# Performance work log

Hardware: AMD Instinct MI355X
Metric: run time of the kernel (lower is better)

## Reference

```python
import jax, jax.numpy as jnp
from jax import lax
import numpy as np

D_MODEL = 1024; N_HEADS = 16; D_K = 64; D_FF = 4096
D_STATE = 16; D_CONV = 4; D_INNER = 2048; EPS = 1e-5
BATCH = 2; SEQ = 2048


def _ln(x, g, b):
    m = x.mean(-1, keepdims=True)
    v = ((x - m) ** 2).mean(-1, keepdims=True)
    return (x - m) * lax.rsqrt(v + EPS) * g + b


def setup_inputs() -> dict:
    key = jax.random.key(0)
    ks = jax.random.split(key, 12)
    rn = lambda k, sh, s=0.02: jax.random.normal(k, sh, jnp.float32) * s
    return {
        'x': jax.random.normal(ks[0], (BATCH, SEQ, D_MODEL), jnp.float32),
        'ln1_g': jnp.ones(D_MODEL), 'ln1_b': jnp.zeros(D_MODEL),
        'Wq': rn(ks[1], (D_MODEL, D_MODEL)), 'bq': jnp.zeros(D_MODEL),
        'Wk': rn(ks[2], (D_MODEL, D_MODEL)), 'bk': jnp.zeros(D_MODEL),
        'Wv': rn(ks[3], (D_MODEL, D_MODEL)), 'bv': jnp.zeros(D_MODEL),
        'Wo': rn(ks[4], (D_MODEL, D_MODEL)), 'bo': jnp.zeros(D_MODEL),
        'ln2_g': jnp.ones(D_MODEL), 'ln2_b': jnp.zeros(D_MODEL),
        'in_w': rn(ks[5], (D_MODEL, 2 * D_INNER)), 'in_b': jnp.zeros(2 * D_INNER),
        'conv_w': rn(ks[6], (D_INNER, 1, D_CONV), 0.2), 'conv_b': jnp.zeros(D_INNER),
        'xp_w': rn(ks[7], (D_INNER, 2 * D_STATE)), 'xp_b': jnp.zeros(2 * D_STATE),
        'dt': rn(ks[8], (D_INNER,), 0.1), 'A': rn(ks[9], (D_STATE, D_STATE), 0.1),
        'Dp': jnp.ones(D_INNER),
        'out_w': rn(ks[10], (D_INNER, D_MODEL)), 'out_b': jnp.zeros(D_MODEL),
        'ln3_g': jnp.ones(D_MODEL), 'ln3_b': jnp.zeros(D_MODEL),
        'fc1_w': rn(ks[11], (D_MODEL, D_FF)), 'fc1_b': jnp.zeros(D_FF),
        'fc2_w': rn(jax.random.fold_in(key, 99), (D_FF, D_MODEL)), 'fc2_b': jnp.zeros(D_MODEL),
    }


def reference(x, ln1_g, ln1_b, Wq, bq, Wk, bk, Wv, bv, Wo, bo, ln2_g, ln2_b,
              in_w, in_b, conv_w, conv_b, xp_w, xp_b, dt, A, Dp, out_w, out_b,
              ln3_g, ln3_b, fc1_w, fc1_b, fc2_w, fc2_b):
    Bsz, S, _ = x.shape
    # --- attention (block sliding-window mask == full causal mask) ---
    h = _ln(x, ln1_g, ln1_b)
    q = (h @ Wq + bq).reshape(Bsz, S, N_HEADS, D_K).transpose(0, 2, 1, 3)
    k = (h @ Wk + bk).reshape(Bsz, S, N_HEADS, D_K).transpose(0, 2, 1, 3)
    v = (h @ Wv + bv).reshape(Bsz, S, N_HEADS, D_K).transpose(0, 2, 1, 3)
    scores = jnp.einsum('bhqd,bhkd->bhqk', q, k) / float(D_K ** 0.5)
    causal = jnp.tril(jnp.ones((S, S), bool))
    scores = jnp.where(causal, scores, -jnp.inf)
    probs = jax.nn.softmax(scores, axis=-1)
    attn = jnp.einsum('bhqk,bhkd->bhqd', probs, v).transpose(0, 2, 1, 3).reshape(Bsz, S, D_MODEL)
    x = x + attn @ Wo + bo
    # --- Mamba-style layer ---
    h = _ln(x, ln2_g, ln2_b)
    xr = h @ in_w + in_b                      # (B,S,2*Di)
    xm, res = xr[..., :D_INNER], xr[..., D_INNER:]
    # causal depthwise conv: torch Conv1d(pad=d_conv-1)[..., :S] == left-pad conv
    xc = lax.conv_general_dilated(xm.transpose(0, 2, 1), conv_w, (1,), [(D_CONV - 1, 0)],
                                  dimension_numbers=('NCH', 'OIH', 'NCH'),
                                  feature_group_count=D_INNER)
    xm = jax.nn.silu((xc + conv_b[None, :, None]).transpose(0, 2, 1))
    xdbl = xm @ xp_w + xp_b                   # (B,S,2*d_state)
    Bm, Cm = xdbl[..., :D_STATE], xdbl[..., D_STATE:]
    # dt = exp(param)[:d_state], indexed by i % d_state per step (as in source)
    dts = jnp.exp(dt)[:D_STATE][jnp.arange(S) % D_STATE]  # (S,)
    # NOTE: the source scan never uses u = x[:,i,:] (and hence D); hs depends
    # only on dt, A, B, C — replicated faithfully here.

    def step(hst, inp):
        d_t, b_t, c_t = inp
        A_t = jnp.exp(d_t * A)                # (d_state,d_state)
        hst = jnp.tanh(hst @ A_t.T) + b_t * hst + c_t
        return hst, hst

    h0 = jnp.zeros((Bsz, D_STATE), x.dtype)
    _, hs = lax.scan(step, h0, (dts, Bm.transpose(1, 0, 2), Cm.transpose(1, 0, 2)))
    hs = hs.transpose(1, 0, 2)                # (B,S,d_state)
    y = jnp.repeat(hs, D_INNER // D_STATE, axis=-1) + res
    x = x + y @ out_w + out_b
    # --- FFN (tanh-approx GELU) ---
    h = _ln(x, ln3_g, ln3_b)
    x = x + jax.nn.gelu(h @ fc1_w + fc1_b, approximate=True) @ fc2_w + fc2_b
    return x
```

## Files before the change

kernel.cpp:

```cpp
#include <hip/hip_runtime.h>
#include <hip/hip_bf16.h>


#define SEQ     2048
#define BATCH   2
#define MROWS   4096
#define DMODEL  1024
#define DINNER  2048
#define DFF     4096
#define QKVLD   3072

typedef __attribute__((ext_vector_type(8))) short bf16x8;
typedef __attribute__((ext_vector_type(4))) float f32x4;
typedef __attribute__((ext_vector_type(2))) __fp16 f16x2;

__device__ __forceinline__ unsigned short f2b(float x){
    __hip_bfloat16 h = __float2bfloat16(x);
    return *reinterpret_cast<unsigned short*>(&h);
}
__device__ __forceinline__ float b2f(unsigned short u){
    __hip_bfloat16 h;
    *reinterpret_cast<unsigned short*>(&h) = u;
    return __bfloat162float(h);
}
__device__ __forceinline__ float gelu_f(float v){
    float u = 0.7978845608f*(v + 0.044715f*v*v*v);
    float e = __expf(2.f*u);
    float th = 1.f - 2.f*__builtin_amdgcn_rcpf(e + 1.f);
    return 0.5f*v*(1.f + th);
}
__device__ __forceinline__ void gload16(const unsigned short* g, unsigned short* l){
    __builtin_amdgcn_global_load_lds(
        (const __attribute__((address_space(1))) void*)g,
        (__attribute__((address_space(3))) void*)l, 16, 0, 0);
}
__device__ __forceinline__ void gload16f(const float* g, float* l){
    __builtin_amdgcn_global_load_lds(
        (const __attribute__((address_space(1))) void*)g,
        (__attribute__((address_space(3))) void*)l, 16, 0, 0);
}
template<int CTRL>
__device__ __forceinline__ float dppf(float x){
    int r = __builtin_amdgcn_mov_dpp(__builtin_bit_cast(int, x), CTRL, 0xf, 0xf, false);
    return __builtin_bit_cast(float, r);
}
template<int CTRL>
__device__ __forceinline__ int dppi(int x){
    return __builtin_amdgcn_mov_dpp(x, CTRL, 0xf, 0xf, false);
}
template<int CTRL>
__device__ __forceinline__ f16x2 dpp_h2(f16x2 x){
    int r = __builtin_amdgcn_mov_dpp(__builtin_bit_cast(int, x), CTRL, 0xf, 0xf, false);
    return __builtin_bit_cast(f16x2, r);
}

#if __has_builtin(__builtin_amdgcn_exp2f)
#define W_SCALE 2.8853900817779268f
__device__ __forceinline__ float exp_2s(float x){ return __builtin_amdgcn_exp2f(x); }
#else
#define W_SCALE 2.0f
__device__ __forceinline__ float exp_2s(float x){ return __expf(x); }
#endif

__device__ __forceinline__ float hdot2(f16x2 a, f16x2 b, float c){
#if __has_builtin(__builtin_amdgcn_fdot2)
    return __builtin_amdgcn_fdot2(a, b, c, false);
#else
    return c + (float)a[0]*(float)b[0] + (float)a[1]*(float)b[1];
#endif
}

__global__ __launch_bounds__(256) void transpose_cast(
    const float* __restrict__ W, unsigned short* __restrict__ Wt, int K, int N)
{
    __shared__ float t[64*65];
    int n0 = blockIdx.x*64, k0 = blockIdx.y*64;
    int c = threadIdx.x & 63, r0 = threadIdx.x >> 6;
    #pragma unroll
    for (int rr = 0; rr < 64; rr += 4)
        t[(rr+r0)*65 + c] = W[(size_t)(k0+rr+r0)*N + n0 + c];
    __syncthreads();
    #pragma unroll
    for (int rr = 0; rr < 64; rr += 4)
        Wt[(size_t)(n0+rr+r0)*K + k0 + c] = f2b(t[c*65 + rr + r0]);
}

__global__ __launch_bounds__(256) void concat_bias(
    const float* __restrict__ b0, const float* __restrict__ b1,
    const float* __restrict__ b2, float* __restrict__ o)
{
    int t = blockIdx.x*256 + threadIdx.x;
    float v = (t < 1024) ? b0[t] : (t < 2048 ? b1[t-1024] : b2[t-2048]);
    o[t] = v;
}

__global__ __launch_bounds__(256) void layernorm_bf16(
    const float* __restrict__ x, const float* __restrict__ g,
    const float* __restrict__ b, unsigned short* __restrict__ out)
{
    int row = blockIdx.x;
    const float4* xr = (const float4*)(x + (size_t)row*DMODEL);
    int tid = threadIdx.x;
    float4 xv = xr[tid];
    float s  = xv.x + xv.y + xv.z + xv.w;
    float ss = xv.x*xv.x + xv.y*xv.y + xv.z*xv.z + xv.w*xv.w;
    #pragma unroll
    for (int d = 32; d > 0; d >>= 1){ s += __shfl_xor(s,d); ss += __shfl_xor(ss,d); }
    __shared__ float sm[8];
    int wv = tid>>6, ln = tid&63;
    if (ln == 0){ sm[wv] = s; sm[4+wv] = ss; }
    __syncthreads();
    s  = sm[0]+sm[1]+sm[2]+sm[3];
    ss = sm[4]+sm[5]+sm[6]+sm[7];
    float mean = s*(1.f/DMODEL);
    float var  = ss*(1.f/DMODEL) - mean*mean;
    float rstd = rsqrtf(var + 1e-5f);
    float4 gv = ((const float4*)g)[tid];
    float4 bv = ((const float4*)b)[tid];
    ushort4 o;
    o.x = f2b((xv.x-mean)*rstd*gv.x + bv.x);
    o.y = f2b((xv.y-mean)*rstd*gv.y + bv.y);
    o.z = f2b((xv.z-mean)*rstd*gv.z + bv.z);
    o.w = f2b((xv.w-mean)*rstd*gv.w + bv.w);
    ((ushort4*)(out + (size_t)row*DMODEL))[tid] = o;
}

template<int BN, int OUT_BF16, int HAS_RES, int ACT>
__global__ __launch_bounds__(256,2) void gemm_bt(
    const unsigned short* __restrict__ A, const unsigned short* __restrict__ Bt,
    const float* __restrict__ bias, const float* __restrict__ res,
    void* __restrict__ outp, int Ndim, int Kdim)
{
    constexpr int NT = BN/32;
    constexpr int BROWS = BN/32;
    __shared__ unsigned short As[128*64];
    __shared__ unsigned short Bs[BN*64];
    int tid = threadIdx.x;
    int lane = tid & 63, wv = tid >> 6;
    int l15 = lane & 15, quad = lane >> 4;
    int m0 = blockIdx.y*128, n0 = blockIdx.x*BN;
    int mo = (wv>>1)*64, no = (wv&1)*(BN/2);
    int rsub = (lane >> 3);
    int cc8  = (lane & 7)*8;
    f32x4 zz = {0.f,0.f,0.f,0.f};
    f32x4 acc[4][NT];
    #pragma unroll
    for (int i=0;i<4;++i)
      #pragma unroll
      for (int j=0;j<NT;++j) acc[i][j] = zz;

    for (int k0 = 0; k0 < Kdim; k0 += 64){
        const unsigned short* Ab = A  + (size_t)(m0 + wv*32 + rsub)*Kdim + k0 + cc8;
        const unsigned short* Bb = Bt + (size_t)(n0 + wv*(BN/4) + rsub)*Kdim + k0 + cc8;
        #pragma unroll
        for (int i=0;i<4;++i)
            gload16(Ab + (size_t)(i*8)*Kdim, &As[(wv*32 + i*8)*64]);
        #pragma unroll
        for (int i=0;i<BROWS;++i)
            gload16(Bb + (size_t)(i*8)*Kdim, &Bs[(wv*(BN/4) + i*8)*64]);
        __syncthreads();
        #pragma unroll
        for (int kc=0;kc<2;++kc){
            bf16x8 af[4], bfr[NT];
            #pragma unroll
            for (int t=0;t<4;++t)
                af[t]  = *(const bf16x8*)(&As[(mo + t*16 + l15)*64 + kc*32 + quad*8]);
            #pragma unroll
            for (int t=0;t<NT;++t)
                bfr[t] = *(const bf16x8*)(&Bs[(no + t*16 + l15)*64 + kc*32 + quad*8]);
            #pragma unroll
            for (int mt=0;mt<4;++mt)
              #pragma unroll
              for (int nt=0;nt<NT;++nt)
                acc[mt][nt] = __builtin_amdgcn_mfma_f32_16x16x32_bf16(af[mt], bfr[nt], acc[mt][nt], 0,0,0);
        }
        __syncthreads();
    }
    #pragma unroll
    for (int mt=0;mt<4;++mt){
      #pragma unroll
      for (int nt=0;nt<NT;++nt){
        int gn = n0 + no + nt*16 + l15;
        float bval = bias[gn];
        #pragma unroll
        for (int r=0;r<4;++r){
            int gm = m0 + mo + mt*16 + quad*4 + r;
            size_t off = (size_t)gm*Ndim + gn;
            float v = acc[mt][nt][r] + bval;
            if constexpr (HAS_RES) v += res[off];
            if constexpr (ACT == 1) v = gelu_f(v);
            if constexpr (OUT_BF16) ((unsigned short*)outp)[off] = f2b(v);
            else                    ((float*)outp)[off] = v;
        }
      }
    }
}

__global__ __launch_bounds__(256) void transpose_v(
    const unsigned short* __restrict__ qkv, unsigned short* __restrict__ vT)
{
    __shared__ unsigned int t[64*33];
    int bh = blockIdx.y;
    int t0 = blockIdx.x*64;
    int tid = threadIdx.x;
    const size_t base = (size_t)(bh>>4)*SEQ*QKVLD + (size_t)(bh&15)*64 + 2*DMODEL;
    #pragma unroll
    for (int i=0;i<2;++i){
        int idx = tid + i*256;
        int r = idx>>3, cc = idx&7;
        uint4 vv = *(const uint4*)(qkv + base + (size_t)(t0+r)*QKVLD + cc*8);
        t[r*33 + cc*4 + 0] = vv.x;
        t[r*33 + cc*4 + 1] = vv.y;
        t[r*33 + cc*4 + 2] = vv.z;
        t[r*33 + cc*4 + 3] = vv.w;
    }
    __syncthreads();
    unsigned short* outb = vT + (size_t)bh*64*SEQ + t0;
    #pragma unroll
    for (int i=0;i<2;++i){
        int idx = tid + i*256;
        int d = idx>>3, cc = idx&7;
        int sh = (d&1)*16, dp = d>>1;
        unsigned int o4[4];
        #pragma unroll
        for (int j2=0;j2<4;++j2){
            unsigned int ua = t[(cc*8 + 2*j2    )*33 + dp];
            unsigned int ub = t[(cc*8 + 2*j2 + 1)*33 + dp];
            unsigned int ha = (ua >> sh) & 0xffff;
            unsigned int hb = (ub >> sh) & 0xffff;
            o4[j2] = ha | (hb << 16);
        }
        *(uint4*)(outb + (size_t)d*SEQ + cc*8) = *(uint4*)o4;
    }
}

__global__ __launch_bounds__(256,2) void attn_flash(
    const unsigned short* __restrict__ qkv, const unsigned short* __restrict__ vT,
    unsigned short* __restrict__ attn)
{
    __shared__ unsigned short Ks[128*72];
    __shared__ unsigned short Vt[64*136];
    __shared__ unsigned short Ps[64*136];
    int bh = blockIdx.y;
    int qt = (int)gridDim.x - 1 - (int)blockIdx.x;
    int q0 = qt*64;
    int tid = threadIdx.x, wv = tid>>6, lane = tid&63;
    int l15 = lane&15, quad = lane>>4;
    const size_t basei = (size_t)(bh>>4)*SEQ*QKVLD + (size_t)(bh&15)*64;
    const unsigned short* q = qkv + basei;
    const unsigned short* k = qkv + basei + DMODEL;
    const unsigned short* vTb = vT + (size_t)bh*64*SEQ;
    const size_t baseo = (size_t)(bh>>4)*SEQ*DMODEL + (size_t)(bh&15)*64;

    bf16x8 aq0 = *(const bf16x8*)(q + (size_t)(q0 + wv*16 + l15)*QKVLD + quad*8);
    bf16x8 aq1 = *(const bf16x8*)(q + (size_t)(q0 + wv*16 + l15)*QKVLD + 32 + quad*8);

    int nkt = (q0 + 191) >> 7;

    uint4 rK[4], rV[4];
    #pragma unroll
    for (int p=0;p<4;++p){
        int c = tid + p*256;
        rK[p] = *(const uint4*)(k   + (size_t)(c>>3)*QKVLD + (c&7)*8);
        rV[p] = *(const uint4*)(vTb + (size_t)(c>>4)*SEQ   + (c&15)*8);
    }

    float m_i[4], l_i[4];
    f32x4 zz = {0.f,0.f,0.f,0.f};
    f32x4 o[4];
    #pragma unroll
    for (int r=0;r<4;++r){ m_i[r] = -__builtin_inff(); l_i[r] = 0.f; }
    #pragma unroll
    for (int d=0;d<4;++d) o[d] = zz;

    for (int kt = 0; kt < nkt; ++kt){
        int t0 = kt*128;
        __syncthreads();
        #pragma unroll
        for (int p=0;p<4;++p){
            int c = tid + p*256;
            *(uint4*)(&Ks[(c>>3)*72  + (c&7)*8])  = rK[p];
            *(uint4*)(&Vt[(c>>4)*136 + (c&15)*8]) = rV[p];
        }
        __syncthreads();
        if (kt + 1 < nkt){
            int t1 = t0 + 128;
            #pragma unroll
            for (int p=0;p<4;++p){
                int c = tid + p*256;
                rK[p] = *(const uint4*)(k   + (size_t)(t1 + (c>>3))*QKVLD + (c&7)*8);
                rV[p] = *(const uint4*)(vTb + (size_t)(c>>4)*SEQ + t1 + (c&15)*8);
            }
        }

        f32x4 sc[8];
        #pragma unroll
        for (int st=0;st<8;++st){
            bf16x8 b0 = *(const bf16x8*)(&Ks[(st*16+l15)*72 + quad*8]);
            bf16x8 b1 = *(const bf16x8*)(&Ks[(st*16+l15)*72 + 32 + quad*8]);
            sc[st] = __builtin_amdgcn_mfma_f32_16x16x32_bf16(aq0, b0, zz, 0,0,0);
            sc[st] = __builtin_amdgcn_mfma_f32_16x16x32_bf16(aq1, b1, sc[st], 0,0,0);
        }
        bool diagt = (kt == nkt-1);
        float mrow[4];
        #pragma unroll
        for (int r=0;r<4;++r) mrow[r] = -__builtin_inff();
        #pragma unroll
        for (int st=0;st<8;++st)
          #pragma unroll
          for (int r=0;r<4;++r){
            float svv = sc[st][r]*0.125f;
            if (diagt && (t0 + st*16 + l15 > q0 + wv*16 + quad*4 + r))
                svv = -__builtin_inff();
            sc[st][r] = svv;
            mrow[r] = fmaxf(mrow[r], svv);
          }
        #pragma unroll
        for (int d=1; d<16; d<<=1)
          #pragma unroll
          for (int r=0;r<4;++r) mrow[r] = fmaxf(mrow[r], __shfl_xor(mrow[r], d));
        float alpha[4], rsum[4];
        #pragma unroll
        for (int r=0;r<4;++r){
            float mn = fmaxf(m_i[r], mrow[r]);
            alpha[r] = __expf(m_i[r] - mn);
            m_i[r] = mn;
        }
        #pragma unroll
        for (int st=0;st<8;++st)
          #pragma unroll
          for (int r=0;r<4;++r) sc[st][r] = __expf(sc[st][r] - m_i[r]);
        #pragma unroll
        for (int r=0;r<4;++r){
            rsum[r] = ((sc[0][r]+sc[1][r])+(sc[2][r]+sc[3][r]))
                    + ((sc[4][r]+sc[5][r])+(sc[6][r]+sc[7][r]));
        }
        #pragma unroll
        for (int d=1; d<16; d<<=1)
          #pragma unroll
          for (int r=0;r<4;++r) rsum[r] += __shfl_xor(rsum[r], d);
        #pragma unroll
        for (int r=0;r<4;++r) l_i[r] = l_i[r]*alpha[r] + rsum[r];
        #pragma unroll
        for (int st=0;st<8;++st)
          #pragma unroll
          for (int r=0;r<4;++r)
            Ps[(wv*16 + quad*4 + r)*136 + st*16 + l15] = f2b(sc[st][r]);
        #pragma unroll
        for (int d=0;d<4;++d)
          #pragma unroll
          for (int r=0;r<4;++r) o[d][r] = o[d][r]*alpha[r];

        bf16x8 ap[4];
        #pragma unroll
        for (int kch=0;kch<4;++kch)
            ap[kch] = *(const bf16x8*)(&Ps[(wv*16 + l15)*136 + kch*32 + quad*8]);
        #pragma unroll
        for (int dtile=0;dtile<4;++dtile){
            #pragma unroll
            for (int kch=0;kch<4;++kch){
                bf16x8 bv_ = *(const bf16x8*)(&Vt[(dtile*16+l15)*136 + kch*32 + quad*8]);
                o[dtile] = __builtin_amdgcn_mfma_f32_16x16x32_bf16(ap[kch], bv_, o[dtile], 0,0,0);
            }
        }
    }
    #pragma unroll
    for (int r=0;r<4;++r){
        float inv = 1.f/l_i[r];
        int gm = q0 + wv*16 + quad*4 + r;
        #pragma unroll
        for (int dtile=0;dtile<4;++dtile)
            attn[baseo + (size_t)gm*DMODEL + dtile*16 + l15] = f2b(o[dtile][r]*inv);
    }
}

__global__ __launch_bounds__(256) void conv_silu(
    const unsigned short* __restrict__ xr, const float* __restrict__ cw,
    const float* __restrict__ cb, unsigned short* __restrict__ xm2)
{
    int idx = blockIdx.x*256 + threadIdx.x;
    int r  = idx >> 10;
    int c2 = (idx & 1023)*2;
    int s  = r & (SEQ-1);
    float4 w0 = *(const float4*)(cw + c2*4);
    float4 w1 = *(const float4*)(cw + (c2+1)*4);
    float w0a[4] = {w0.x,w0.y,w0.z,w0.w};
    float w1a[4] = {w1.x,w1.y,w1.z,w1.w};
    float a0 = cb[c2], a1 = cb[c2+1];
    const unsigned short* xrow = xr + (size_t)r*DFF + c2;
    #pragma unroll
    for (int j=0;j<4;++j){
        int sp = s - 3 + j;
        if (sp >= 0){
            int off = (j-3)*DFF;
            unsigned int u = *(const unsigned int*)(xrow + off);
            a0 += w0a[j]*b2f(u & 0xffff);
            a1 += w1a[j]*b2f(u >> 16);
        }
    }
    float s0 = a0 * __builtin_amdgcn_rcpf(1.f + __expf(-a0));
    float s1 = a1 * __builtin_amdgcn_rcpf(1.f + __expf(-a1));
    unsigned int op = (unsigned int)f2b(s0) | ((unsigned int)f2b(s1) << 16);
    *(unsigned int*)(xm2 + (size_t)r*DINNER + c2) = op;
}

__global__ __launch_bounds__(256) void xp_gemm(
    const unsigned short* __restrict__ xm2, const float* __restrict__ w,
    const float* __restrict__ bias, float* __restrict__ xdbl)
{
    int tid = threadIdx.x;
    int lr = tid >> 5, n = tid & 31;
    int row = blockIdx.x*8 + lr;
    const unsigned short* ar = xm2 + (size_t)row*DINNER;
    float acc = bias[n];
    #pragma unroll 4
    for (int k2 = 0; k2 < DINNER; k2 += 2){
        unsigned int u = *(const unsigned int*)(ar + k2);
        acc += b2f(u & 0xffff)*w[k2*32 + n] + b2f(u >> 16)*w[(k2+1)*32 + n];
    }
    int nc = (n < 16) ? 2*n : 2*(n-16)+1;
    xdbl[(size_t)row*32 + nc] = acc;
}

__device__ __forceinline__ float scan_step_dot(float h, const f16x2 (&Wp)[8],
                                               float bv, float cv)
{
    float rr = dppf<0x121>(h);
    f16x2 p0 = __builtin_amdgcn_cvt_pkrtz(h, rr);
    f16x2 p1 = dpp_h2<0x122>(p0);
    f16x2 p2 = dpp_h2<0x124>(p0);
    f16x2 p3 = dpp_h2<0x126>(p0);
    f16x2 p4 = dpp_h2<0x128>(p0);
    f16x2 p5 = dpp_h2<0x12a>(p0);
    f16x2 p6 = dpp_h2<0x12c>(p0);
    f16x2 p7 = dpp_h2<0x12e>(p0);
    float a0 = hdot2(Wp[0], p0, 0.f);
    a0 = hdot2(Wp[1], p1, a0);
    a0 = hdot2(Wp[2], p2, a0);
    a0 = hdot2(Wp[3], p3, a0);
    float a1 = hdot2(Wp[4], p4, 0.f);
    a1 = hdot2(Wp[5], p5, a1);
    a1 = hdot2(Wp[6], p6, a1);
    a1 = hdot2(Wp[7], p7, a1);
    float u  = fmaf(bv, h, cv + 1.f);
    float e2 = exp_2s(a0 + a1);
    float r  = __builtin_amdgcn_rcpf(e2 + 1.f);
    return fmaf(-2.f, r, u);
}

__device__ __forceinline__ void load_bank(float2 (&bk)[16], const float* src){
    #pragma unroll
    for (int j=0;j<16;++j) bk[j] = *(const float2*)(src + (size_t)j*32);
}

__device__ __forceinline__ void compute16(const float2 (&bk)[16],
                                          const f16x2 (&Wf)[16][8],
                                          float& hn, float* hp, int lane)
{
    float h0s=0.f, h1s=0.f, h2s=0.f;
    #pragma unroll
    for (int j=0;j<16;++j){
        hn = scan_step_dot(hn, Wf[j], bk[j].x, bk[j].y);
        if ((j&3)==0)      h0s = hn;
        else if ((j&3)==1) h1s = hn;
        else if ((j&3)==2) h2s = hn;
        else if (lane < 16){
            float4 o4 = {h0s, h1s, h2s, hn};
            *(float4*)(hp + j - 3) = o4;
        }
    }
}

__global__ __launch_bounds__(128,1) void scan_k(
    const float* __restrict__ xdbl, const float* __restrict__ dt,
    const float* __restrict__ A, float* __restrict__ hsT)
{
    int tid = threadIdx.x;
    int lane = tid & 63;
    int b = tid >> 6;
    int i = lane & 15;

    int c1 = dppi<0x121>(i);
    int sj[8], tj[8];
    sj[0] = i;               tj[0] = c1;
    sj[1] = dppi<0x122>(i);  tj[1] = dppi<0x122>(c1);
    sj[2] = dppi<0x124>(i);  tj[2] = dppi<0x124>(c1);
    sj[3] = dppi<0x126>(i);  tj[3] = dppi<0x126>(c1);
    sj[4] = dppi<0x128>(i);  tj[4] = dppi<0x128>(c1);
    sj[5] = dppi<0x12a>(i);  tj[5] = dppi<0x12a>(c1);
    sj[6] = dppi<0x12c>(i);  tj[6] = dppi<0x12c>(c1);
    sj[7] = dppi<0x12e>(i);  tj[7] = dppi<0x12e>(c1);

    f16x2 Wf[16][8];
    #pragma unroll
    for (int p=0;p<16;++p){
        float dtp = __expf(dt[p]);
        #pragma unroll
        for (int jj=0;jj<8;++jj){
            float w0 = W_SCALE*__expf(dtp * A[i*16 + sj[jj]]);
            float w1 = W_SCALE*__expf(dtp * A[i*16 + tj[jj]]);
            Wf[p][jj] = __builtin_amdgcn_cvt_pkrtz(w0, w1);
        }
    }

    const float* src = xdbl + (size_t)(b*SEQ)*32 + 2*i;
    float* hp = hsT + (size_t)(b*16 + i)*SEQ;
    float2 bA[16], bB[16];
    load_bank(bA, src);
    float hn = 0.f;
    for (int bp = 0; bp < 64; ++bp){
        int t0 = bp*32;
        load_bank(bB, src + (size_t)(t0+16)*32);
        compute16(bA, Wf, hn, hp + t0, lane);
        int t2 = (bp < 63) ? (t0 + 32) : 0;
        load_bank(bA, src + (size_t)t2*32);
        compute16(bB, Wf, hn, hp + t0 + 16, lane);
    }
}

__global__ __launch_bounds__(256) void y_assemble(
    const float* __restrict__ hsT, const unsigned short* __restrict__ xr,
    unsigned short* __restrict__ y)
{
    int idx = blockIdx.x*256 + threadIdx.x;
    int r = idx >> 10;
    int c2 = (idx & 1023)*2;
    int bb = r >> 11, s = r & (SEQ-1);
    unsigned int u = *(const unsigned int*)(xr + (size_t)r*DFF + DINNER + c2);
    float h0 = hsT[(size_t)(bb*16 + (c2 >> 7))*SEQ + s];
    float y0 = h0 + b2f(u & 0xffff);
    float y1 = h0 + b2f(u >> 16);
    *(unsigned int*)(y + (size_t)r*DINNER + c2) =
        (unsigned int)f2b(y0) | ((unsigned int)f2b(y1) << 16);
}

extern "C" void kernel_launch(void* const* d_in, const int* in_sizes, int n_in,
                              void* d_out, int out_size, void* d_ws, size_t ws_size,
                              hipStream_t stream)
{
    (void)in_sizes; (void)n_in; (void)out_size; (void)ws_size;
    const float* x     = (const float*)d_in[0];
    const float* ln1_g = (const float*)d_in[1];
    const float* ln1_b = (const float*)d_in[2];
    const float* Wq    = (const float*)d_in[3];
    const float* bq    = (const float*)d_in[4];
    const float* Wk    = (const float*)d_in[5];
    const float* bk    = (const float*)d_in[6];
    const float* Wv    = (const float*)d_in[7];
    const float* bv    = (const float*)d_in[8];
    const float* Wo    = (const float*)d_in[9];
    const float* bo    = (const float*)d_in[10];
    const float* ln2_g = (const float*)d_in[11];
    const float* ln2_b = (const float*)d_in[12];
    const float* in_w  = (const float*)d_in[13];
    const float* in_b  = (const float*)d_in[14];
    const float* conv_w= (const float*)d_in[15];
    const float* conv_b= (const float*)d_in[16];
    const float* xp_w  = (const float*)d_in[17];
    const float* xp_b  = (const float*)d_in[18];
    const float* dt    = (const float*)d_in[19];
    const float* A     = (const float*)d_in[20];
    const float* out_w = (const float*)d_in[22];
    const float* out_b = (const float*)d_in[23];
    const float* ln3_g = (const float*)d_in[24];
    const float* ln3_b = (const float*)d_in[25];
    const float* fc1_w = (const float*)d_in[26];
    const float* fc1_b = (const float*)d_in[27];
    const float* fc2_w = (const float*)d_in[28];
    const float* fc2_b = (const float*)d_in[29];

    char* ws = (char*)d_ws;
    const size_t MB = 1ull << 20;
    unsigned short* qkvT = (unsigned short*)(ws + 0*MB);
    unsigned short* WoT  = (unsigned short*)(ws + 6*MB);
    unsigned short* inT  = (unsigned short*)(ws + 8*MB);
    unsigned short* outT = (unsigned short*)(ws + 16*MB);
    unsigned short* f1T  = (unsigned short*)(ws + 20*MB);
    unsigned short* f2T  = (unsigned short*)(ws + 28*MB);
    unsigned short* hbf  = (unsigned short*)(ws + 36*MB);
    float*          x2   = (float*)(ws + 44*MB);
    float*          x3   = (float*)(ws + 60*MB);
    unsigned short* qkv  = (unsigned short*)(ws + 76*MB);
    unsigned short* attnb= (unsigned short*)(ws + 100*MB);
    unsigned short* xr   = (unsigned short*)(ws + 76*MB);
    unsigned short* ffn  = (unsigned short*)(ws + 76*MB);
    unsigned short* xm2  = (unsigned short*)(ws + 108*MB);
    unsigned short* yb   = (unsigned short*)(ws + 108*MB);
    float*          xdbl = (float*)(ws + 124*MB);
    float*          hsb  = (float*)(ws + 124*MB + 512*1024);
    float*          bqkv = (float*)(ws + 125*MB);

    dim3 blk(256);
    transpose_cast<<<dim3(16,16), blk, 0, stream>>>(Wq, qkvT,              1024, 1024);
    transpose_cast<<<dim3(16,16), blk, 0, stream>>>(Wk, qkvT + 1024*1024,  1024, 1024);
    transpose_cast<<<dim3(16,16), blk, 0, stream>>>(Wv, qkvT + 2*1024*1024,1024, 1024);
    transpose_cast<<<dim3(16,16), blk, 0, stream>>>(Wo, WoT, 1024, 1024);
    transpose_cast<<<dim3(64,16), blk, 0, stream>>>(in_w, inT, 1024, 4096);
    transpose_cast<<<dim3(16,32), blk, 0, stream>>>(out_w, outT, 2048, 1024);
    transpose_cast<<<dim3(64,16), blk, 0, stream>>>(fc1_w, f1T, 1024, 4096);
    transpose_cast<<<dim3(16,64), blk, 0, stream>>>(fc2_w, f2T, 4096, 1024);
    concat_bias<<<12, blk, 0, stream>>>(bq, bk, bv, bqkv);

    layernorm_bf16<<<MROWS, blk, 0, stream>>>(x, ln1_g, ln1_b, hbf);
    gemm_bt<128,1,0,0><<<dim3(24,32), blk, 0, stream>>>(hbf, qkvT, bqkv, nullptr, qkv, QKVLD, 1024);
    transpose_v<<<dim3(32,32), blk, 0, stream>>>(qkv, hbf);
    attn_flash<<<dim3(32,32), blk, 0, stream>>>(qkv, hbf, attnb);
    gemm_bt<64,0,1,0><<<dim3(16,32), blk, 0, stream>>>(attnb, WoT, bo, x, x2, 1024, 1024);
    layernorm_bf16<<<MROWS, blk, 0, stream>>>(x2, ln2_g, ln2_b, hbf);
    gemm_bt<128,1,0,0><<<dim3(32,32), blk, 0, stream>>>(hbf, inT, in_b, nullptr, xr, 4096, 1024);
    conv_silu<<<16384, blk, 0, stream>>>(xr, conv_w, conv_b, xm2);
    xp_gemm<<<512, blk, 0, stream>>>(xm2, xp_w, xp_b, xdbl);
    scan_k<<<1, dim3(128), 0, stream>>>(xdbl, dt, A, hsb);
    y_assemble<<<16384, blk, 0, stream>>>(hsb, xr, yb);
    gemm_bt<64,0,1,0><<<dim3(16,32), blk, 0, stream>>>(yb, outT, out_b, x2, x3, 1024, 2048);
    layernorm_bf16<<<MROWS, blk, 0, stream>>>(x3, ln3_g, ln3_b, hbf);
    gemm_bt<128,1,0,1><<<dim3(32,32), blk, 0, stream>>>(hbf, f1T, fc1_b, nullptr, ffn, 4096, 1024);
    gemm_bt<64,0,1,0><<<dim3(16,32), blk, 0, stream>>>(ffn, f2T, fc2_b, x3, (float*)d_out, 1024, 4096);
}
```

Before: 938.7 us.

## Stage attention K/V with direct global-to-LDS loads into XOR-swizzled tiles

The flash-attention kernel now loads K and V^T tiles straight into LDS with global_load_lds, using an XOR swizzle instead of padded rows. This replaces the old register prefetch-then-store path and frees registers, so launch bounds rise to three blocks per CU. Scores are prescaled by log2(e) so a base-2 exponential can be used. The next tile is now loaded only after the current tile's compute, between two barriers, so overlap within a block is lost; hiding that load latency now depends on the extra occupancy.

```diff
diff --git a/kernel.cpp b/kernel.cpp
--- a/kernel.cpp
+++ b/kernel.cpp
@@ -30,11 +30,6 @@
     return 0.5f*v*(1.f + th);
 }
 __device__ __forceinline__ void gload16(const unsigned short* g, unsigned short* l){
-    __builtin_amdgcn_global_load_lds(
-        (const __attribute__((address_space(1))) void*)g,
-        (__attribute__((address_space(3))) void*)l, 16, 0, 0);
-}
-__device__ __forceinline__ void gload16f(const float* g, float* l){
     __builtin_amdgcn_global_load_lds(
         (const __attribute__((address_space(1))) void*)g,
         (__attribute__((address_space(3))) void*)l, 16, 0, 0);
@@ -234,36 +229,46 @@
     }
 }
 
-__global__ __launch_bounds__(256,2) void attn_flash(
+__device__ __forceinline__ void stage_kv(
+    const unsigned short* __restrict__ k, const unsigned short* __restrict__ vTb,
+    int t0, unsigned short* Ks, unsigned short* Vt, int wv, int lane)
+{
+    #pragma unroll
+    for (int p=0;p<4;++p){
+        int c0 = p*256 + wv*64;
+        int c  = c0 + lane;
+        int kr = c>>3, kc = (c&7)*8;
+        int vr = c>>4, vc = (c&15)*8;
+        gload16(k   + (size_t)(t0+kr)*QKVLD + (kc ^ ((kr&7)<<3)), Ks + c0*8);
+        gload16(vTb + (size_t)vr*SEQ + t0 +   (vc ^ ((vr&7)<<3)), Vt + c0*8);
+    }
+}
+
+__global__ __launch_bounds__(256,3) void attn_flash(
     const unsigned short* __restrict__ qkv, const unsigned short* __restrict__ vT,
     unsigned short* __restrict__ attn)
 {
-    __shared__ unsigned short Ks[128*72];
-    __shared__ unsigned short Vt[64*136];
+    __shared__ unsigned short Ks[128*64];
+    __shared__ unsigned short Vt[64*128];
     __shared__ unsigned short Ps[64*136];
     int bh = blockIdx.y;
     int qt = (int)gridDim.x - 1 - (int)blockIdx.x;
     int q0 = qt*64;
     int tid = threadIdx.x, wv = tid>>6, lane = tid&63;
     int l15 = lane&15, quad = lane>>4;
+    int xsw = (l15&7)<<3;
     const size_t basei = (size_t)(bh>>4)*SEQ*QKVLD + (size_t)(bh&15)*64;
     const unsigned short* q = qkv + basei;
     const unsigned short* k = qkv + basei + DMODEL;
     const unsigned short* vTb = vT + (size_t)bh*64*SEQ;
     const size_t baseo = (size_t)(bh>>4)*SEQ*DMODEL + (size_t)(bh&15)*64;
 
+    int nkt = (q0 + 191) >> 7;
+
+    stage_kv(k, vTb, 0, Ks, Vt, wv, lane);
+
     bf16x8 aq0 = *(const bf16x8*)(q + (size_t)(q0 + wv*16 + l15)*QKVLD + quad*8);
     bf16x8 aq1 = *(const bf16x8*)(q + (size_t)(q0 + wv*16 + l15)*QKVLD + 32 + quad*8);
-
-    int nkt = (q0 + 191) >> 7;
-
-    uint4 rK[4], rV[4];
-    #pragma unroll
-    for (int p=0;p<4;++p){
-        int c = tid + p*256;
-        rK[p] = *(const uint4*)(k   + (size_t)(c>>3)*QKVLD + (c&7)*8);
-        rV[p] = *(const uint4*)(vTb + (size_t)(c>>4)*SEQ   + (c&15)*8);
-    }
 
     float m_i[4], l_i[4];
     f32x4 zz = {0.f,0.f,0.f,0.f};
@@ -273,31 +278,18 @@
     #pragma unroll
     for (int d=0;d<4;++d) o[d] = zz;
 
+    const float SCL = 0.1803368801111137f;
+
+    __syncthreads();
+
     for (int kt = 0; kt < nkt; ++kt){
         int t0 = kt*128;
-        __syncthreads();
-        #pragma unroll
-        for (int p=0;p<4;++p){
-            int c = tid + p*256;
-            *(uint4*)(&Ks[(c>>3)*72  + (c&7)*8])  = rK[p];
-            *(uint4*)(&Vt[(c>>4)*136 + (c&15)*8]) = rV[p];
-        }
-        __syncthreads();
-        if (kt + 1 < nkt){
-            int t1 = t0 + 128;
-            #pragma unroll
-            for (int p=0;p<4;++p){
-                int c = tid + p*256;
-                rK[p] = *(const uint4*)(k   + (size_t)(t1 + (c>>3))*QKVLD + (c&7)*8);
-                rV[p] = *(const uint4*)(vTb + (size_t)(c>>4)*SEQ + t1 + (c&15)*8);
-            }
-        }
 
         f32x4 sc[8];
         #pragma unroll
         for (int st=0;st<8;++st){
-            bf16x8 b0 = *(const bf16x8*)(&Ks[(st*16+l15)*72 + quad*8]);
-            bf16x8 b1 = *(const bf16x8*)(&Ks[(st*16+l15)*72 + 32 + quad*8]);
+            bf16x8 b0 = *(const bf16x8*)(&Ks[(st*16+l15)*64 + ((     quad*8) ^ xsw)]);
+            bf16x8 b1 = *(const bf16x8*)(&Ks[(st*16+l15)*64 + ((32 + quad*8) ^ xsw)]);
             sc[st] = __builtin_amdgcn_mfma_f32_16x16x32_bf16(aq0, b0, zz, 0,0,0);
             sc[st] = __builtin_amdgcn_mfma_f32_16x16x32_bf16(aq1, b1, sc[st], 0,0,0);
         }
@@ -309,7 +301,7 @@
         for (int st=0;st<8;++st)
           #pragma unroll
           for (int r=0;r<4;++r){
-            float svv = sc[st][r]*0.125f;
+            float svv = sc[st][r]*SCL;
             if (diagt && (t0 + st*16 + l15 > q0 + wv*16 + quad*4 + r))
                 svv = -__builtin_inff();
             sc[st][r] = svv;
@@ -323,13 +315,13 @@
         #pragma unroll
         for (int r=0;r<4;++r){
             float mn = fmaxf(m_i[r], mrow[r]);
-            alpha[r] = __expf(m_i[r] - mn);
+            alpha[r] = exp_2s(m_i[r] - mn);
             m_i[r] = mn;
         }
         #pragma unroll
         for (int st=0;st<8;++st)
           #pragma unroll
-          for (int r=0;r<4;++r) sc[st][r] = __expf(sc[st][r] - m_i[r]);
+          for (int r=0;r<4;++r) sc[st][r] = exp_2s(sc[st][r] - m_i[r]);
         #pragma unroll
         for (int r=0;r<4;++r){
             rsum[r] = ((sc[0][r]+sc[1][r])+(sc[2][r]+sc[3][r]))
@@ -359,9 +351,15 @@
         for (int dtile=0;dtile<4;++dtile){
             #pragma unroll
             for (int kch=0;kch<4;++kch){
-                bf16x8 bv_ = *(const bf16x8*)(&Vt[(dtile*16+l15)*136 + kch*32 + quad*8]);
+                bf16x8 bv_ = *(const bf16x8*)(&Vt[(dtile*16+l15)*128 + ((kch*32 + quad*8) ^ xsw)]);
                 o[dtile] = __builtin_amdgcn_mfma_f32_16x16x32_bf16(ap[kch], bv_, o[dtile], 0,0,0);
             }
+        }
+
+        if (kt + 1 < nkt){
+            __syncthreads();
+            stage_kv(k, vTb, t0 + 128, Ks, Vt, wv, lane);
+            __syncthreads();
         }
     }
     #pragma unroll
```

Measured after the change: 863.8 us. 8.0% less time.
